# Performance work log

Measured on AMD Instinct MI355X. Metric: run time of the kernel, lower is better.

The kernel has to match this reference:

```python
import jax, jax.numpy as jnp
import numpy as np

B, N_IN, HID, N_OUT = 1024, 512, 64, 256


def setup_inputs() -> dict:
    key = jax.random.key(0)
    ks = jax.random.split(key, 10)
    s = 0.02
    return {
        "x": jax.random.normal(ks[0], (B, N_IN), dtype=jnp.float32),
        "ln_gamma": jnp.ones((N_IN,), dtype=jnp.float32),
        "ln_beta": jnp.zeros((N_IN,), dtype=jnp.float32),
        "Wq": jax.random.normal(ks[1], (N_IN, HID * N_OUT), dtype=jnp.float32) * s,
        "bq": jnp.zeros((HID * N_OUT,), dtype=jnp.float32),
        "Wk": jax.random.normal(ks[2], (N_IN, HID * N_OUT), dtype=jnp.float32) * s,
        "bk": jnp.zeros((HID * N_OUT,), dtype=jnp.float32),
        "Wv": jax.random.normal(ks[3], (N_IN, HID * N_OUT), dtype=jnp.float32) * s,
        "bv": jnp.zeros((HID * N_OUT,), dtype=jnp.float32),
        "Wo": jax.random.normal(ks[4], (HID, N_OUT), dtype=jnp.float32) * s,
        "bo": jnp.zeros((N_OUT,), dtype=jnp.float32),
    }


def reference(x, ln_gamma, ln_beta, Wq, bq, Wk, bk, Wv, bv, Wo, bo):
    # LayerNorm over last dim (input_shape)
    mu = jnp.mean(x, axis=-1, keepdims=True)
    var = jnp.mean(jnp.square(x - mu), axis=-1, keepdims=True)
    h = (x - mu) / jnp.sqrt(var + 1e-5) * ln_gamma + ln_beta  # (B, 512)

    # QKV projections, then view as (B, N_OUT, HID)
    q = (h @ Wq + bq).reshape(B, N_OUT, HID)
    k = (h @ Wk + bk).reshape(B, N_OUT, HID)
    v = (h @ Wv + bv).reshape(B, N_OUT, HID)

    # Single-head scaled dot-product attention over length N_OUT
    w = jnp.einsum("bqc,bkc->bqk", q, k) * (HID ** -0.5)
    w = jax.nn.softmax(w, axis=2)
    a = jnp.einsum("bqk,bkc->bqc", w, v)  # (B, N_OUT, HID)

    # Output projection, ReLU, negate -> seminegative contact map
    out = jax.nn.relu(a @ Wo + bo)  # (B, N_OUT, N_OUT)
    return -out
```

## Files before the change

kernel.cpp:

```cpp
#include <hip/hip_runtime.h>
#include <hip/hip_fp16.h>

typedef _Float16 h4_t __attribute__((ext_vector_type(4)));
typedef _Float16 h8_t __attribute__((ext_vector_type(8)));
typedef float f4_t __attribute__((ext_vector_type(4)));

#define B_SZ 1024
#define N_IN 512
#define HID 64
#define N_OUT 256
#define QKN (N_OUT * HID)

__global__ __launch_bounds__(256) void k_ln(const float* __restrict__ x,
                                            const float* __restrict__ gamma,
                                            const float* __restrict__ beta,
                                            _Float16* __restrict__ h16) {
    int tid = threadIdx.x;
    int wave = tid >> 6, lane = tid & 63;
    int row = blockIdx.x * 4 + wave;
    const float4* xr = (const float4*)(x + (size_t)row * N_IN);
    float4 a = xr[lane];
    float4 b = xr[lane + 64];
    float s = a.x + a.y + a.z + a.w + b.x + b.y + b.z + b.w;
    float sq = a.x * a.x + a.y * a.y + a.z * a.z + a.w * a.w +
               b.x * b.x + b.y * b.y + b.z * b.z + b.w * b.w;
    for (int off = 1; off < 64; off <<= 1) {
        s += __shfl_xor(s, off);
        sq += __shfl_xor(sq, off);
    }
    float mean = s * (1.0f / N_IN);
    float var = sq * (1.0f / N_IN) - mean * mean;
    float rstd = rsqrtf(var + 1e-5f);
    float4 g0 = ((const float4*)gamma)[lane];
    float4 g1 = ((const float4*)gamma)[lane + 64];
    float4 e0 = ((const float4*)beta)[lane];
    float4 e1 = ((const float4*)beta)[lane + 64];
    h4_t o0 = {(_Float16)((a.x - mean) * rstd * g0.x + e0.x),
               (_Float16)((a.y - mean) * rstd * g0.y + e0.y),
               (_Float16)((a.z - mean) * rstd * g0.z + e0.z),
               (_Float16)((a.w - mean) * rstd * g0.w + e0.w)};
    h4_t o1 = {(_Float16)((b.x - mean) * rstd * g1.x + e1.x),
               (_Float16)((b.y - mean) * rstd * g1.y + e1.y),
               (_Float16)((b.z - mean) * rstd * g1.z + e1.z),
               (_Float16)((b.w - mean) * rstd * g1.w + e1.w)};
    h4_t* hr = (h4_t*)(h16 + (size_t)row * N_IN);
    hr[lane] = o0;
    hr[lane + 64] = o1;
}

__global__ __launch_bounds__(256) void k_wt(const float* __restrict__ Wq,
                                            const float* __restrict__ Wk,
                                            const float* __restrict__ Wv,
                                            _Float16* __restrict__ wt) {
    __shared__ _Float16 t[64][65];
    const float* W = blockIdx.z == 0 ? Wq : (blockIdx.z == 1 ? Wk : Wv);
    _Float16* out = wt + (size_t)blockIdx.z * ((size_t)QKN * N_IN);
    int n0 = blockIdx.x * 64, k0 = blockIdx.y * 64;
    int c = threadIdx.x & 63, rq = threadIdx.x >> 6;
    for (int i = 0; i < 16; i++) {
        int r = i * 4 + rq;
        t[r][c] = (_Float16)W[(size_t)(k0 + r) * QKN + n0 + c];
    }
    __syncthreads();
    for (int i = 0; i < 16; i++) {
        int r = i * 4 + rq;
        out[(size_t)(n0 + r) * N_IN + k0 + c] = t[c][r];
    }
}

__global__ __launch_bounds__(256) void k_qkv(const _Float16* __restrict__ h16,
                                             const _Float16* __restrict__ wt,
                                             const float* __restrict__ bq,
                                             const float* __restrict__ bk,
                                             const float* __restrict__ bv,
                                             _Float16* __restrict__ qkv) {
    __shared__ _Float16 As[128 * 32];
    __shared__ _Float16 Bs[128 * 32];
    int z = blockIdx.z;
    const _Float16* Wb = wt + (size_t)z * ((size_t)QKN * N_IN);
    const float* bias = z == 0 ? bq : (z == 1 ? bk : bv);
    _Float16* out = qkv + (size_t)z * ((size_t)B_SZ * QKN);
    int m0 = blockIdx.x * 128, n0 = blockIdx.y * 128;
    int tid = threadIdx.x, lane = tid & 63, w = tid >> 6;
    int wm = w & 1, wn = w >> 1;
    int col16 = lane & 15, quad = lane >> 4;
    f4_t acc[4][4] = {};
    for (int kk = 0; kk < N_IN; kk += 32) {
        __syncthreads();
        for (int c = 0; c < 2; c++) {
            int idx = (w * 2 + c) * 512 + lane * 8;
            int row = idx >> 5, col = idx & 31;
            __builtin_amdgcn_global_load_lds(
                (const __attribute__((address_space(1))) void*)(h16 + (size_t)(m0 + row) * N_IN + kk + col),
                (__attribute__((address_space(3))) void*)(As + (w * 2 + c) * 512),
                16, 0, 0);
            __builtin_amdgcn_global_load_lds(
                (const __attribute__((address_space(1))) void*)(Wb + (size_t)(n0 + row) * N_IN + kk + col),
                (__attribute__((address_space(3))) void*)(Bs + (w * 2 + c) * 512),
                16, 0, 0);
        }
        __syncthreads();
        h8_t af[4], bf[4];
        for (int mt = 0; mt < 4; mt++)
            af[mt] = *(const h8_t*)(As + (wm * 64 + mt * 16 + col16) * 32 + quad * 8);
        for (int nt = 0; nt < 4; nt++)
            bf[nt] = *(const h8_t*)(Bs + (wn * 64 + nt * 16 + col16) * 32 + quad * 8);
        for (int mt = 0; mt < 4; mt++)
            for (int nt = 0; nt < 4; nt++)
                acc[mt][nt] = __builtin_amdgcn_mfma_f32_16x16x32_f16(af[mt], bf[nt], acc[mt][nt], 0, 0, 0);
    }
    for (int nt = 0; nt < 4; nt++) {
        int n = n0 + wn * 64 + nt * 16 + col16;
        float bb = bias[n];
        for (int mt = 0; mt < 4; mt++) {
            int mbase = m0 + wm * 64 + mt * 16 + quad * 4;
            for (int r = 0; r < 4; r++)
                out[(size_t)(mbase + r) * QKN + n] = (_Float16)(acc[mt][nt][r] + bb);
        }
    }
}

__global__ __launch_bounds__(256) void k_attn(const _Float16* __restrict__ qkv,
                                              const float* __restrict__ Wo,
                                              const float* __restrict__ bo,
                                              float* __restrict__ out) {
    __shared__ _Float16 lds[32768];
    int b = blockIdx.x;
    int tid = threadIdx.x, lane = tid & 63, w = tid >> 6;
    int col16 = lane & 15, quad = lane >> 4;
    const _Float16* qb = qkv + (size_t)b * QKN;
    const _Float16* kb = qkv + (size_t)(B_SZ + b) * QKN;
    const _Float16* vb = qkv + (size_t)(2 * B_SZ + b) * QKN;

    {
        int i = tid & 7;
        int kb0 = tid >> 3;
        for (int it = 0; it < 8; it++) {
            int key = kb0 + it * 32;
            h4_t ka = *(const h4_t*)(kb + key * 64 + i * 8);
            h4_t kc2 = *(const h4_t*)(kb + key * 64 + i * 8 + 4);
            *(h4_t*)(lds + (2 * i) * 1024 + key * 4) = ka;
            *(h4_t*)(lds + (2 * i + 1) * 1024 + key * 4) = kc2;
            const _Float16* vp = vb + key * 64 + i * 8;
            _Float16* vt = lds + 16384 + (key >> 2) * 256 + (key & 3);
            for (int j = 0; j < 8; j++) vt[(i * 8 + j) * 4] = vp[j];
        }
    }
    __syncthreads();

    h4_t qf[4][4];
    int qbase = w * 64;
    for (int qt = 0; qt < 4; qt++)
        for (int ki = 0; ki < 4; ki++)
            qf[qt][ki] = *(const h4_t*)(qb + (qbase + qt * 16 + col16) * 64 + ki * 16 + quad * 4);

    f4_t o[4][4] = {};
    float mrun[4], lrun[4];
    for (int qt = 0; qt < 4; qt++) { mrun[qt] = -1e30f; lrun[qt] = 0.f; }
    const float sc = 0.125f * 1.44269504088896f;

    for (int kc = 0; kc < 16; kc++) {
        h4_t kf[4];
        for (int ki = 0; ki < 4; ki++)
            kf[ki] = *(const h4_t*)(lds + (ki * 4 + quad) * 1024 + (kc * 16 + col16) * 4);
        f4_t st[4];
        for (int qt = 0; qt < 4; qt++) {
            f4_t a = {};
            for (int ki = 0; ki < 4; ki++)
                a = __builtin_amdgcn_mfma_f32_16x16x16f16(kf[ki], qf[qt][ki], a, 0, 0, 0);
            st[qt] = a;
        }
        h4_t vf[4];
        for (int mt = 0; mt < 4; mt++)
            vf[mt] = *(const h4_t*)(lds + 16384 + (kc * 4 + quad) * 256 + (mt * 16 + col16) * 4);
        for (int qt = 0; qt < 4; qt++) {
            float s0 = st[qt][0] * sc, s1 = st[qt][1] * sc;
            float s2 = st[qt][2] * sc, s3 = st[qt][3] * sc;
            float cm = fmaxf(fmaxf(s0, s1), fmaxf(s2, s3));
            cm = fmaxf(cm, __shfl_xor(cm, 16));
            cm = fmaxf(cm, __shfl_xor(cm, 32));
            float mnew = fmaxf(mrun[qt], cm);
            float alpha = exp2f(mrun[qt] - mnew);
            float p0 = exp2f(s0 - mnew), p1 = exp2f(s1 - mnew);
            float p2 = exp2f(s2 - mnew), p3 = exp2f(s3 - mnew);
            float ps = p0 + p1 + p2 + p3;
            ps += __shfl_xor(ps, 16);
            ps += __shfl_xor(ps, 32);
            lrun[qt] = lrun[qt] * alpha + ps;
            mrun[qt] = mnew;
            h4_t pf = {(_Float16)p0, (_Float16)p1, (_Float16)p2, (_Float16)p3};
            for (int mt = 0; mt < 4; mt++) {
                f4_t t = o[mt][qt];
                t[0] *= alpha; t[1] *= alpha; t[2] *= alpha; t[3] *= alpha;
                o[mt][qt] = __builtin_amdgcn_mfma_f32_16x16x16f16(vf[mt], pf, t, 0, 0, 0);
            }
        }
    }

    h4_t af[4][4];
    for (int qt = 0; qt < 4; qt++) {
        float rl = 1.0f / lrun[qt];
        for (int hk = 0; hk < 4; hk++) {
            f4_t t = o[hk][qt];
            af[qt][hk] = (h4_t){(_Float16)(t[0] * rl), (_Float16)(t[1] * rl),
                                (_Float16)(t[2] * rl), (_Float16)(t[3] * rl)};
        }
    }
    __syncthreads();
    for (int it = 0; it < 64; it++) {
        int f = it * 256 + tid;
        int hh = f >> 8, no = f & 255;
        lds[(hh >> 2) * 1024 + no * 4 + (hh & 3)] = (_Float16)Wo[f];
    }
    __syncthreads();

    float* outb = out + (size_t)b * (N_OUT * N_OUT);
    for (int nc = 0; nc < 4; nc++) {
        for (int nt = 0; nt < 4; nt++) {
            int no = nc * 64 + nt * 16 + col16;
            h4_t wf[4];
            for (int hk = 0; hk < 4; hk++)
                wf[hk] = *(const h4_t*)(lds + (hk * 4 + quad) * 1024 + no * 4);
            float bb = bo[no];
            for (int qt = 0; qt < 4; qt++) {
                f4_t a = {};
                for (int hk = 0; hk < 4; hk++)
                    a = __builtin_amdgcn_mfma_f32_16x16x16f16(af[qt][hk], wf[hk], a, 0, 0, 0);
                int qrow = qbase + qt * 16 + quad * 4;
                for (int r = 0; r < 4; r++) {
                    float v = a[r] + bb;
                    outb[(size_t)(qrow + r) * N_OUT + no] = (v > 0.f) ? -v : 0.f;
                }
            }
        }
    }
}

extern "C" void kernel_launch(void* const* d_in, const int* in_sizes, int n_in,
                              void* d_out, int out_size, void* d_ws, size_t ws_size,
                              hipStream_t stream) {
    const float* x = (const float*)d_in[0];
    const float* gamma = (const float*)d_in[1];
    const float* beta = (const float*)d_in[2];
    const float* Wq = (const float*)d_in[3];
    const float* bq = (const float*)d_in[4];
    const float* Wk = (const float*)d_in[5];
    const float* bk = (const float*)d_in[6];
    const float* Wv = (const float*)d_in[7];
    const float* bv = (const float*)d_in[8];
    const float* Wo = (const float*)d_in[9];
    const float* bo = (const float*)d_in[10];
    float* out = (float*)d_out;

    _Float16* h16 = (_Float16*)d_ws;
    _Float16* wt16 = h16 + (size_t)B_SZ * N_IN;
    _Float16* qkv16 = wt16 + (size_t)3 * QKN * N_IN;

    k_ln<<<dim3(B_SZ / 4), 256, 0, stream>>>(x, gamma, beta, h16);
    k_wt<<<dim3(QKN / 64, N_IN / 64, 3), 256, 0, stream>>>(Wq, Wk, Wv, wt16);
    k_qkv<<<dim3(B_SZ / 128, QKN / 128, 3), 256, 0, stream>>>(h16, wt16, bq, bk, bv, qkv16);
    k_attn<<<dim3(B_SZ), 256, 0, stream>>>(qkv16, Wo, bo, out);
}
```

Before: 518.5 us.

## Pipeline V loads via double-buffered LDS, async K load, lazy softmax rescale

The attention kernel now loads K straight into LDS with global_load_lds and uses 16x16x32 MFMAs for QK^T. V is transposed into a double-buffered, XOR-swizzled LDS region in four chunks, with the next chunk's global loads issued before the current chunk's compute. The online softmax skips the rescale of the running max and output whenever the new scores stay within a threshold of the old max, and the Wo staging writes packed h4 stores. This cuts LDS footprint, bank conflicts and VALU rescale work, at the cost of more barriers and added complexity.

```diff
diff --git a/kernel.cpp b/kernel.cpp
--- a/kernel.cpp
+++ b/kernel.cpp
@@ -124,7 +124,7 @@
                                               const float* __restrict__ Wo,
                                               const float* __restrict__ bo,
                                               float* __restrict__ out) {
-    __shared__ _Float16 lds[32768];
+    __shared__ _Float16 lds[24576];
     int b = blockIdx.x;
     int tid = threadIdx.x, lane = tid & 63, w = tid >> 6;
     int col16 = lane & 15, quad = lane >> 4;
@@ -132,68 +132,97 @@
     const _Float16* kb = qkv + (size_t)(B_SZ + b) * QKN;
     const _Float16* vb = qkv + (size_t)(2 * B_SZ + b) * QKN;
 
-    {
-        int i = tid & 7;
-        int kb0 = tid >> 3;
-        for (int it = 0; it < 8; it++) {
-            int key = kb0 + it * 32;
-            h4_t ka = *(const h4_t*)(kb + key * 64 + i * 8);
-            h4_t kc2 = *(const h4_t*)(kb + key * 64 + i * 8 + 4);
-            *(h4_t*)(lds + (2 * i) * 1024 + key * 4) = ka;
-            *(h4_t*)(lds + (2 * i + 1) * 1024 + key * 4) = kc2;
-            const _Float16* vp = vb + key * 64 + i * 8;
-            _Float16* vt = lds + 16384 + (key >> 2) * 256 + (key & 3);
-            for (int j = 0; j < 8; j++) vt[(i * 8 + j) * 4] = vp[j];
-        }
-    }
-    __syncthreads();
-
-    h4_t qf[4][4];
+    for (int r = 0; r < 8; r++) {
+        int slab = r * 4 + w;
+        int c8 = slab >> 2, kblk = slab & 3;
+        __builtin_amdgcn_global_load_lds(
+            (const __attribute__((address_space(1))) void*)(kb + (size_t)(kblk * 64 + lane) * 64 + c8 * 8),
+            (__attribute__((address_space(3))) void*)(lds + slab * 512),
+            16, 0, 0);
+    }
+
+    int kq = lane >> 2, k3 = lane & 3, kx = kq & 7;
+    h8_t v0a = *(const h8_t*)(vb + (size_t)lane * 64 + w * 16);
+    h8_t v0b = *(const h8_t*)(vb + (size_t)lane * 64 + w * 16 + 8);
+
+    h8_t qf[4][2];
     int qbase = w * 64;
     for (int qt = 0; qt < 4; qt++)
-        for (int ki = 0; ki < 4; ki++)
-            qf[qt][ki] = *(const h4_t*)(qb + (qbase + qt * 16 + col16) * 64 + ki * 16 + quad * 4);
+        for (int ki = 0; ki < 2; ki++)
+            qf[qt][ki] = *(const h8_t*)(qb + (size_t)(qbase + qt * 16 + col16) * 64 + ki * 32 + quad * 8);
+
+    {
+        _Float16* vp = lds + 16384 + kq * 256 + k3;
+        for (int j = 0; j < 8; j++) vp[(size_t)((w * 16 + j) ^ kx) * 4] = v0a[j];
+        for (int j = 0; j < 8; j++) vp[(size_t)((w * 16 + 8 + j) ^ kx) * 4] = v0b[j];
+    }
+    __syncthreads();
 
     f4_t o[4][4] = {};
     float mrun[4], lrun[4];
     for (int qt = 0; qt < 4; qt++) { mrun[qt] = -1e30f; lrun[qt] = 0.f; }
-    const float sc = 0.125f * 1.44269504088896f;
-
-    for (int kc = 0; kc < 16; kc++) {
-        h4_t kf[4];
-        for (int ki = 0; ki < 4; ki++)
-            kf[ki] = *(const h4_t*)(lds + (ki * 4 + quad) * 1024 + (kc * 16 + col16) * 4);
-        f4_t st[4];
-        for (int qt = 0; qt < 4; qt++) {
-            f4_t a = {};
-            for (int ki = 0; ki < 4; ki++)
-                a = __builtin_amdgcn_mfma_f32_16x16x16f16(kf[ki], qf[qt][ki], a, 0, 0, 0);
-            st[qt] = a;
-        }
-        h4_t vf[4];
-        for (int mt = 0; mt < 4; mt++)
-            vf[mt] = *(const h4_t*)(lds + 16384 + (kc * 4 + quad) * 256 + (mt * 16 + col16) * 4);
-        for (int qt = 0; qt < 4; qt++) {
-            float s0 = st[qt][0] * sc, s1 = st[qt][1] * sc;
-            float s2 = st[qt][2] * sc, s3 = st[qt][3] * sc;
-            float cm = fmaxf(fmaxf(s0, s1), fmaxf(s2, s3));
-            cm = fmaxf(cm, __shfl_xor(cm, 16));
-            cm = fmaxf(cm, __shfl_xor(cm, 32));
-            float mnew = fmaxf(mrun[qt], cm);
-            float alpha = exp2f(mrun[qt] - mnew);
-            float p0 = exp2f(s0 - mnew), p1 = exp2f(s1 - mnew);
-            float p2 = exp2f(s2 - mnew), p3 = exp2f(s3 - mnew);
-            float ps = p0 + p1 + p2 + p3;
-            ps += __shfl_xor(ps, 16);
-            ps += __shfl_xor(ps, 32);
-            lrun[qt] = lrun[qt] * alpha + ps;
-            mrun[qt] = mnew;
-            h4_t pf = {(_Float16)p0, (_Float16)p1, (_Float16)p2, (_Float16)p3};
-            for (int mt = 0; mt < 4; mt++) {
-                f4_t t = o[mt][qt];
-                t[0] *= alpha; t[1] *= alpha; t[2] *= alpha; t[3] *= alpha;
-                o[mt][qt] = __builtin_amdgcn_mfma_f32_16x16x16f16(vf[mt], pf, t, 0, 0, 0);
+    const float sc = 0.125f * 1.44269504f;
+
+    for (int chunk = 0; chunk < 4; chunk++) {
+        int buf = chunk & 1;
+        h8_t vna, vnb;
+        if (chunk < 3) {
+            vna = *(const h8_t*)(vb + (size_t)((chunk + 1) * 64 + lane) * 64 + w * 16);
+            vnb = *(const h8_t*)(vb + (size_t)((chunk + 1) * 64 + lane) * 64 + w * 16 + 8);
+        }
+        for (int kc4 = 0; kc4 < 4; kc4++) {
+            int kc = chunk * 4 + kc4;
+            h8_t kf0 = *(const h8_t*)(lds + (size_t)(quad)*2048 + (size_t)(kc * 16 + col16) * 8);
+            h8_t kf1 = *(const h8_t*)(lds + (size_t)(4 + quad) * 2048 + (size_t)(kc * 16 + col16) * 8);
+            int kqr = kc4 * 4 + quad, kxr = kqr & 7;
+            h4_t vf[4];
+            for (int mt = 0; mt < 4; mt++)
+                vf[mt] = *(const h4_t*)(lds + 16384 + buf * 4096 + kqr * 256 +
+                                        (size_t)((mt * 16 + col16) ^ kxr) * 4);
+            for (int qt = 0; qt < 4; qt++) {
+                f4_t s = {};
+                __builtin_amdgcn_s_setprio(1);
+                s = __builtin_amdgcn_mfma_f32_16x16x32_f16(kf0, qf[qt][0], s, 0, 0, 0);
+                s = __builtin_amdgcn_mfma_f32_16x16x32_f16(kf1, qf[qt][1], s, 0, 0, 0);
+                __builtin_amdgcn_s_setprio(0);
+                float cm = fmaxf(fmaxf(s[0], s[1]), fmaxf(s[2], s[3]));
+                cm = fmaxf(cm, __shfl_xor(cm, 16));
+                cm = fmaxf(cm, __shfl_xor(cm, 32));
+                float m0 = mrun[qt];
+                bool defer = __all(cm <= m0 + 44.0f) != 0;
+                float mn = defer ? m0 : fmaxf(m0, cm);
+                float msc = mn * sc;
+                float p0 = exp2f(__builtin_fmaf(s[0], sc, -msc));
+                float p1 = exp2f(__builtin_fmaf(s[1], sc, -msc));
+                float p2 = exp2f(__builtin_fmaf(s[2], sc, -msc));
+                float p3 = exp2f(__builtin_fmaf(s[3], sc, -msc));
+                float ps = p0 + p1 + p2 + p3;
+                ps += __shfl_xor(ps, 16);
+                ps += __shfl_xor(ps, 32);
+                if (defer) {
+                    lrun[qt] += ps;
+                } else {
+                    float alpha = exp2f((m0 - mn) * sc);
+                    lrun[qt] = lrun[qt] * alpha + ps;
+                    mrun[qt] = mn;
+                    for (int mt = 0; mt < 4; mt++) {
+                        f4_t t = o[mt][qt];
+                        t[0] *= alpha; t[1] *= alpha; t[2] *= alpha; t[3] *= alpha;
+                        o[mt][qt] = t;
+                    }
+                }
+                h4_t pf = {(_Float16)p0, (_Float16)p1, (_Float16)p2, (_Float16)p3};
+                __builtin_amdgcn_s_setprio(1);
+                for (int mt = 0; mt < 4; mt++)
+                    o[mt][qt] = __builtin_amdgcn_mfma_f32_16x16x16f16(vf[mt], pf, o[mt][qt], 0, 0, 0);
+                __builtin_amdgcn_s_setprio(0);
             }
+        }
+        if (chunk < 3) {
+            _Float16* vp = lds + 16384 + (buf ^ 1) * 4096 + kq * 256 + k3;
+            for (int j = 0; j < 8; j++) vp[(size_t)((w * 16 + j) ^ kx) * 4] = vna[j];
+            for (int j = 0; j < 8; j++) vp[(size_t)((w * 16 + 8 + j) ^ kx) * 4] = vnb[j];
+            __syncthreads();
         }
     }
 
@@ -207,10 +236,12 @@
         }
     }
     __syncthreads();
-    for (int it = 0; it < 64; it++) {
-        int f = it * 256 + tid;
-        int hh = f >> 8, no = f & 255;
-        lds[(hh >> 2) * 1024 + no * 4 + (hh & 3)] = (_Float16)Wo[f];
+    for (int it = 0; it < 16; it++) {
+        h4_t wv = {(_Float16)Wo[(size_t)(it * 4 + 0) * 256 + tid],
+                   (_Float16)Wo[(size_t)(it * 4 + 1) * 256 + tid],
+                   (_Float16)Wo[(size_t)(it * 4 + 2) * 256 + tid],
+                   (_Float16)Wo[(size_t)(it * 4 + 3) * 256 + tid]};
+        *(h4_t*)(lds + it * 1024 + tid * 4) = wv;
     }
     __syncthreads();
 
@@ -224,8 +255,10 @@
             float bb = bo[no];
             for (int qt = 0; qt < 4; qt++) {
                 f4_t a = {};
+                __builtin_amdgcn_s_setprio(1);
                 for (int hk = 0; hk < 4; hk++)
                     a = __builtin_amdgcn_mfma_f32_16x16x16f16(af[qt][hk], wf[hk], a, 0, 0, 0);
+                __builtin_amdgcn_s_setprio(0);
                 int qrow = qbase + qt * 16 + quad * 4;
                 for (int r = 0; r < 4; r++) {
                     float v = a[r] + bb;
```

Result: slower. 586.8 us (+13.2%).
